# Optimization experiments

Measured on AMD Instinct MI355X. Metric: run time of the kernel, lower is better.

The kernel has to match this reference:

```python
import jax, jax.numpy as jnp
import numpy as np

EMBED_DIM = 1024
BATCH = 4
SEQ = 2048


def setup_inputs() -> dict:
    key = jax.random.key(0)
    ks = jax.random.split(key, 9)
    E = EMBED_DIM
    s = 1.0 / np.sqrt(E)
    inp = {
        "x": jax.random.normal(ks[0], (BATCH, SEQ, E), dtype=jnp.float32),
        "Wq": jax.random.uniform(ks[1], (E, E), jnp.float32, -s, s),
        "bq": jax.random.uniform(ks[2], (E,), jnp.float32, -s, s),
        "Wk": jax.random.uniform(ks[3], (E, E), jnp.float32, -s, s),
        "bk": jax.random.uniform(ks[4], (E,), jnp.float32, -s, s),
        "Wv": jax.random.uniform(ks[5], (E, E), jnp.float32, -s, s),
        "bv": jax.random.uniform(ks[6], (E,), jnp.float32, -s, s),
        "Wo": jax.random.uniform(ks[7], (E, E), jnp.float32, -s, s),
        "bo": jax.random.uniform(ks[8], (E,), jnp.float32, -s, s),
    }
    return inp


def reference(x, Wq, bq, Wk, bk, Wv, bv, Wo, bo):
    # x: [B, S, E]. Single-head attention over full embed_dim.
    scale = x.shape[-1] ** -0.5
    q = jnp.einsum("bse,ef->bsf", x, Wq.T) + bq
    k = jnp.einsum("bse,ef->bsf", x, Wk.T) + bk
    v = jnp.einsum("bse,ef->bsf", x, Wv.T) + bv
    scores = jnp.einsum("bqe,bke->bqk", q, k) * scale  # [B, S, S]
    attn = jax.nn.softmax(scores, axis=-1)             # dropout p=0 -> identity
    out = jnp.einsum("bqk,bke->bqe", attn, v)
    return jnp.einsum("bse,ef->bsf", out, Wo.T) + bo
```

## Files before the change

### kernel.cpp

```cpp
#include <hip/hip_runtime.h>
#include <hip/hip_bf16.h>


typedef __bf16 bf16_t;
typedef __bf16 bf16x8 __attribute__((ext_vector_type(8)));
typedef __bf16 bf16x4 __attribute__((ext_vector_type(4)));
typedef float  f32x16 __attribute__((ext_vector_type(16)));

__device__ __forceinline__ void async_copy16(const void* g, void* l) {
  __builtin_amdgcn_global_load_lds(
      (const __attribute__((address_space(1))) void*)g,
      (__attribute__((address_space(3))) void*)l, 16, 0, 0);
}

__device__ __forceinline__ void store_out(float* p, float v)  { *p = v; }
__device__ __forceinline__ void store_out(bf16_t* p, float v) { *p = (bf16_t)v; }

#define BM 128
#define BN 128
#define BKT 64

template <typename OutT, int NBIAS>
__global__ __launch_bounds__(256) void gemm_bt(
    const bf16_t* __restrict__ A, const bf16_t* __restrict__ B,
    OutT* __restrict__ C,
    const float* __restrict__ b0, const float* __restrict__ b1,
    const float* __restrict__ b2,
    int M, int N, int K, int lda, int ldb, int ldc, float scale,
    long long strideA, long long strideB, long long strideC) {
  const int z = blockIdx.z;
  A += (long long)z * strideA;
  B += (long long)z * strideB;
  C += (long long)z * strideC;

  int bx = blockIdx.x, by = blockIdx.y;
  {
    const int GX  = gridDim.x;
    const int id  = by * GX + bx;
    const int per = GX * 8;
    const int grp = id / per;
    const int rem = id - grp * per;
    by = grp * 8 + (rem & 7);
    bx = rem >> 3;
  }

  __shared__ __align__(16) bf16_t As[BM * BKT];
  __shared__ __align__(16) bf16_t Bs[BN * BKT];

  const int t    = threadIdx.x;
  const int lane = t & 63;
  const int w    = t >> 6;
  const int wm   = w & 1;
  const int wn   = w >> 1;
  const int tileM = by * BM;
  const int tileN = bx * BN;

  f32x16 acc[2][2] = {};

  for (int k0 = 0; k0 < K; k0 += BKT) {
#pragma unroll
    for (int i = 0; i < 4; ++i) {
      const int c   = t + 256 * i;
      const int row = c >> 3;
      const int cc  = c & 7;
      const int gcc = cc ^ (row & 7);
      const int ldsbase = ((t & ~63) + 256 * i) * 8;
      async_copy16(A + (long long)(tileM + row) * lda + k0 + gcc * 8, &As[ldsbase]);
      async_copy16(B + (long long)(tileN + row) * ldb + k0 + gcc * 8, &Bs[ldsbase]);
    }
    __syncthreads();

#pragma unroll
    for (int s = 0; s < 4; ++s) {
      const int kc = s + 4 * (lane >> 5);
      bf16x8 af[2], bfr[2];
#pragma unroll
      for (int ti = 0; ti < 2; ++ti) {
        const int row = wm * 64 + ti * 32 + (lane & 31);
        af[ti] = *(const bf16x8*)&As[row * BKT + ((kc ^ (row & 7)) * 8)];
      }
#pragma unroll
      for (int tj = 0; tj < 2; ++tj) {
        const int row = wn * 64 + tj * 32 + (lane & 31);
        bfr[tj] = *(const bf16x8*)&Bs[row * BKT + ((kc ^ (row & 7)) * 8)];
      }
#pragma unroll
      for (int ti = 0; ti < 2; ++ti)
#pragma unroll
        for (int tj = 0; tj < 2; ++tj)
          acc[ti][tj] = __builtin_amdgcn_mfma_f32_32x32x16_bf16(
              af[ti], bfr[tj], acc[ti][tj], 0, 0, 0);
    }
    __syncthreads();
  }

#pragma unroll
  for (int tj = 0; tj < 2; ++tj) {
    const int col = tileN + wn * 64 + tj * 32 + (lane & 31);
    float bv = 0.f;
    if (NBIAS == 1) bv = b0[col];
    if (NBIAS == 3) {
      const float* bp = col < 1024 ? b0 : (col < 2048 ? b1 : b2);
      bv = bp[col & 1023];
    }
#pragma unroll
    for (int ti = 0; ti < 2; ++ti) {
      const int rowb = tileM + wm * 64 + ti * 32 + 4 * (lane >> 5);
#pragma unroll
      for (int r = 0; r < 16; ++r) {
        const int row = rowb + (r & 3) + 8 * (r >> 2);
        store_out(&C[(long long)row * ldc + col], acc[ti][tj][r] * scale + bv);
      }
    }
  }
}

__global__ __launch_bounds__(256) void cast_all(
    const float4* __restrict__ w0, const float4* __restrict__ w1,
    const float4* __restrict__ w2, const float4* __restrict__ w3,
    const float4* __restrict__ x,
    bf16x4* __restrict__ wdst, bf16x4* __restrict__ xdst) {
  const int N4W = 1 << 18;
  const int id = blockIdx.x * 256 + threadIdx.x;
  const float4* src;
  bf16x4* dst;
  if (id < 4 * N4W) {
    const int z = id >> 18;
    src = (z == 0 ? w0 : z == 1 ? w1 : z == 2 ? w2 : w3) + (id & (N4W - 1));
    dst = wdst + id;
  } else {
    const int i = id - 4 * N4W;
    src = x + i;
    dst = xdst + i;
  }
  const float4 v = *src;
  bf16x4 o;
  o[0] = (bf16_t)v.x; o[1] = (bf16_t)v.y; o[2] = (bf16_t)v.z; o[3] = (bf16_t)v.w;
  *dst = o;
}

__global__ __launch_bounds__(256) void transpose_bf16(
    const bf16_t* __restrict__ in, bf16_t* __restrict__ out, int R, int C,
    int ldin, long long sIn, long long sOut) {
  in  += (long long)blockIdx.z * sIn;
  out += (long long)blockIdx.z * sOut;
  __shared__ bf16_t tile[32][33];
  const int tx = threadIdx.x, ty = threadIdx.y;
  const int x = blockIdx.x * 32 + tx;
  const int y0 = blockIdx.y * 32;
#pragma unroll
  for (int j = 0; j < 32; j += 8)
    tile[ty + j][tx] = in[(long long)(y0 + ty + j) * ldin + x];
  __syncthreads();
  const int x2 = y0 + tx;
  const int y2 = blockIdx.x * 32;
#pragma unroll
  for (int j = 0; j < 32; j += 8)
    out[(long long)(y2 + ty + j) * R + x2] = tile[tx][ty + j];
}

__global__ __launch_bounds__(256) void softmax_rows(
    const bf16_t* __restrict__ S, bf16_t* __restrict__ P, int cols) {
  const long long row = blockIdx.x;
  const bf16x8* inp = (const bf16x8*)(S + row * cols);
  bf16x8* outp      = (bf16x8*)(P + row * cols);
  const int t = threadIdx.x;
  const int w = t >> 6, lane = t & 63;

  const bf16x8 v = inp[t];
  float f[8];
#pragma unroll
  for (int j = 0; j < 8; ++j) f[j] = (float)v[j];

  float m = f[0];
#pragma unroll
  for (int j = 1; j < 8; ++j) m = fmaxf(m, f[j]);
#pragma unroll
  for (int off = 32; off > 0; off >>= 1) m = fmaxf(m, __shfl_xor(m, off));

  __shared__ float red[8];
  if (lane == 0) red[w] = m;
  __syncthreads();
  m = fmaxf(fmaxf(red[0], red[1]), fmaxf(red[2], red[3]));

  float e[8], sum = 0.f;
#pragma unroll
  for (int j = 0; j < 8; ++j) { e[j] = __expf(f[j] - m); sum += e[j]; }
#pragma unroll
  for (int off = 32; off > 0; off >>= 1) sum += __shfl_xor(sum, off);
  if (lane == 0) red[4 + w] = sum;
  __syncthreads();
  sum = red[4] + red[5] + red[6] + red[7];

  const float inv = 1.f / sum;
  bf16x8 o;
#pragma unroll
  for (int j = 0; j < 8; ++j) o[j] = (bf16_t)(e[j] * inv);
  outp[t] = o;
}

extern "C" void kernel_launch(void* const* d_in, const int* in_sizes, int n_in,
                              void* d_out, int out_size, void* d_ws, size_t ws_size,
                              hipStream_t stream) {
  const int E = 1024, S = 2048, B = 4;
  const int BS = B * S;

  const float* x  = (const float*)d_in[0];
  const float* Wq = (const float*)d_in[1];
  const float* bq = (const float*)d_in[2];
  const float* Wk = (const float*)d_in[3];
  const float* bk = (const float*)d_in[4];
  const float* Wv = (const float*)d_in[5];
  const float* bv = (const float*)d_in[6];
  const float* Wo = (const float*)d_in[7];
  const float* bo = (const float*)d_in[8];
  float* out = (float*)d_out;

  char* w = (char*)d_ws;
  const size_t MB = 1ull << 20;
  bf16_t* Wqkvb = (bf16_t*)(w + 0 * MB);
  bf16_t* Wob   = Wqkvb + 3 * E * E;
  bf16_t* xb    = (bf16_t*)(w + 8 * MB);
  bf16_t* QKVb  = (bf16_t*)(w + 24 * MB);
  bf16_t* VTb   = (bf16_t*)(w + 72 * MB);
  bf16_t* Sb    = (bf16_t*)(w + 88 * MB);
  bf16_t* Pb    = (bf16_t*)(w + 8 * MB);
  bf16_t* Ob    = (bf16_t*)(w + 40 * MB);

  {
    const int totalBlocks = ((4 << 18) + (1 << 21)) / 256;
    cast_all<<<totalBlocks, 256, 0, stream>>>(
        (const float4*)Wq, (const float4*)Wk, (const float4*)Wv,
        (const float4*)Wo, (const float4*)x, (bf16x4*)Wqkvb, (bf16x4*)xb);
  }

  gemm_bt<bf16_t, 3><<<dim3(3 * E / BN, BS / BM, 1), 256, 0, stream>>>(
      xb, Wqkvb, QKVb, bq, bk, bv,
      BS, 3 * E, E, E, E, 3 * E, 1.f, 0, 0, 0);

  transpose_bf16<<<dim3(E / 32, S / 32, B), dim3(32, 8), 0, stream>>>(
      QKVb + 2 * E, VTb, S, E, 3 * E, (long long)S * 3 * E, (long long)E * S);

  gemm_bt<bf16_t, 0><<<dim3(S / BN, S / BM, B), 256, 0, stream>>>(
      QKVb, QKVb + E, Sb, nullptr, nullptr, nullptr,
      S, S, E, 3 * E, 3 * E, S, 0.03125f,
      (long long)S * 3 * E, (long long)S * 3 * E, (long long)S * S);

  softmax_rows<<<BS, 256, 0, stream>>>(Sb, Pb, S);

  gemm_bt<bf16_t, 0><<<dim3(E / BN, S / BM, B), 256, 0, stream>>>(
      Pb, VTb, Ob, nullptr, nullptr, nullptr,
      S, E, S, S, S, E, 1.f,
      (long long)S * S, (long long)E * S, (long long)S * E);

  gemm_bt<float, 1><<<dim3(E / BN, BS / BM, 1), 256, 0, stream>>>(
      Ob, Wob, out, bo, nullptr, nullptr,
      BS, E, E, E, E, E, 1.f, 0, 0, 0);
}
```

Before: 302.2 us.

## Add 256x256 eight-wave double-buffered GEMM for QKV projection and QK^T

Adds a new GEMM kernel with 256x256 output tiles, 512 threads and 16x16x32 bf16 MFMAs. It double-buffers A and B tiles in LDS through async global-to-LDS copies, with explicit vmcnt waits. The inner loop is split into four MFMA phases separated by barriers, interleaves the next tile's loads between them, and raises wave priority around the MFMA bursts. The goal is more data reuse per tile and less exposed load latency for the two largest GEMMs. In exchange it uses about 128KB of LDS, so only one block fits per CU, and the grids become smaller (384 and 256 blocks), which may underfill the GPU.

```diff
diff --git a/kernel.cpp b/kernel.cpp
--- a/kernel.cpp
+++ b/kernel.cpp
@@ -6,6 +6,7 @@
 typedef __bf16 bf16x8 __attribute__((ext_vector_type(8)));
 typedef __bf16 bf16x4 __attribute__((ext_vector_type(4)));
 typedef float  f32x16 __attribute__((ext_vector_type(16)));
+typedef float  f32x4  __attribute__((ext_vector_type(4)));
 
 __device__ __forceinline__ void async_copy16(const void* g, void* l) {
   __builtin_amdgcn_global_load_lds(
@@ -13,12 +14,193 @@
       (__attribute__((address_space(3))) void*)l, 16, 0, 0);
 }
 
+__device__ __forceinline__ void wg_barrier() {
+  asm volatile("" ::: "memory");
+  __builtin_amdgcn_s_barrier();
+  asm volatile("" ::: "memory");
+}
+
+__device__ __forceinline__ f32x4 mfma16(bf16x8 a, bf16x8 b, f32x4 c) {
+  return __builtin_amdgcn_mfma_f32_16x16x32_bf16(a, b, c, 0, 0, 0);
+}
+
 __device__ __forceinline__ void store_out(float* p, float v)  { *p = v; }
 __device__ __forceinline__ void store_out(bf16_t* p, float v) { *p = (bf16_t)v; }
 
 #define BM 128
 #define BN 128
 #define BKT 64
+
+template <typename OutT, int NBIAS>
+__global__ __launch_bounds__(512, 2) void gemm256_bt(
+    const bf16_t* __restrict__ A, const bf16_t* __restrict__ B,
+    OutT* __restrict__ C,
+    const float* __restrict__ b0, const float* __restrict__ b1,
+    const float* __restrict__ b2,
+    int M, int N, int K, int lda, int ldb, int ldc, float scale,
+    long long strideA, long long strideB, long long strideC) {
+  const int z = blockIdx.z;
+  A += (long long)z * strideA;
+  B += (long long)z * strideB;
+  C += (long long)z * strideC;
+
+  int bx = blockIdx.x, by = blockIdx.y;
+  {
+    const int GX  = gridDim.x;
+    const int id  = by * GX + bx;
+    const int per = GX * 8;
+    const int grp = id / per;
+    const int rem = id - grp * per;
+    by = grp * 8 + (rem & 7);
+    bx = rem >> 3;
+  }
+
+  __shared__ __align__(16) bf16_t As[2 * 256 * 64];
+  __shared__ __align__(16) bf16_t Bs[2 * 256 * 64];
+
+  const int t    = threadIdx.x;
+  const int lane = t & 63;
+  const int w    = t >> 6;
+  const int wm   = w & 1;
+  const int wn   = w >> 1;
+  const int g    = lane >> 4;
+  const int l7   = lane & 7;
+  const int r15  = lane & 15;
+  const int tileM = by * 256;
+  const int tileN = bx * 256;
+
+  const int row0 = t >> 3;
+  const int gcc  = (t & 7) ^ (row0 & 7);
+  const int dstb = (t & ~63) * 8;
+
+  const int sw0 = ((0 + g) ^ l7) * 8;
+  const int sw1 = ((4 + g) ^ l7) * 8;
+  const int aRow = (wm * 128 + r15) * 64;
+  const int bRow = (wn * 64 + r15) * 64;
+
+  const int NT = K >> 6;
+
+  f32x4 acc[8][4] = {};
+
+  auto stageA = [&](int kt, int h) {
+    const int cb = (kt & 1) * 16384;
+    const bf16_t* src =
+        A + (long long)(tileM + h * 128 + row0) * lda + kt * 64 + gcc * 8;
+    bf16_t* dst = &As[cb + h * 8192 + dstb];
+    async_copy16(src, dst);
+    async_copy16(src + (long long)64 * lda, dst + 4096);
+  };
+  auto stageB = [&](int kt, int h) {
+    const int cb = (kt & 1) * 16384;
+    const bf16_t* src =
+        B + (long long)(tileN + h * 128 + row0) * ldb + kt * 64 + gcc * 8;
+    bf16_t* dst = &Bs[cb + h * 8192 + dstb];
+    async_copy16(src, dst);
+    async_copy16(src + (long long)64 * ldb, dst + 4096);
+  };
+
+  stageA(0, 0); stageA(0, 1); stageB(0, 0); stageB(0, 1);
+  stageA(1, 0); stageA(1, 1); stageB(1, 0); stageB(1, 1);
+  asm volatile("s_waitcnt vmcnt(8)" ::: "memory");
+  wg_barrier();
+
+  bf16x8 a[4][2], bq[2][2][2];
+
+  for (int kt = 0; kt < NT; ++kt) {
+    const int cb = (kt & 1) * 16384;
+    const int k2 = kt + 2;
+
+#pragma unroll
+    for (int i = 0; i < 4; ++i) {
+      a[i][0] = *(const bf16x8*)&As[cb + aRow + i * 1024 + sw0];
+      a[i][1] = *(const bf16x8*)&As[cb + aRow + i * 1024 + sw1];
+    }
+#pragma unroll
+    for (int j = 0; j < 2; ++j) {
+      bq[0][j][0] = *(const bf16x8*)&Bs[cb + bRow + j * 1024 + sw0];
+      bq[0][j][1] = *(const bf16x8*)&Bs[cb + bRow + j * 1024 + sw1];
+    }
+    wg_barrier();
+    __builtin_amdgcn_s_setprio(1);
+#pragma unroll
+    for (int i = 0; i < 4; ++i)
+#pragma unroll
+      for (int j = 0; j < 2; ++j) {
+        acc[i][j] = mfma16(a[i][0], bq[0][j][0], acc[i][j]);
+        acc[i][j] = mfma16(a[i][1], bq[0][j][1], acc[i][j]);
+      }
+    __builtin_amdgcn_s_setprio(0);
+    wg_barrier();
+
+#pragma unroll
+    for (int j = 0; j < 2; ++j) {
+      bq[1][j][0] = *(const bf16x8*)&Bs[cb + bRow + 2048 + j * 1024 + sw0];
+      bq[1][j][1] = *(const bf16x8*)&Bs[cb + bRow + 2048 + j * 1024 + sw1];
+    }
+    wg_barrier();
+    __builtin_amdgcn_s_setprio(1);
+#pragma unroll
+    for (int i = 0; i < 4; ++i)
+#pragma unroll
+      for (int j = 0; j < 2; ++j) {
+        acc[i][2 + j] = mfma16(a[i][0], bq[1][j][0], acc[i][2 + j]);
+        acc[i][2 + j] = mfma16(a[i][1], bq[1][j][1], acc[i][2 + j]);
+      }
+    __builtin_amdgcn_s_setprio(0);
+    wg_barrier();
+
+#pragma unroll
+    for (int i = 0; i < 4; ++i) {
+      a[i][0] = *(const bf16x8*)&As[cb + aRow + 4096 + i * 1024 + sw0];
+      a[i][1] = *(const bf16x8*)&As[cb + aRow + 4096 + i * 1024 + sw1];
+    }
+    if (k2 < NT) { stageB(k2, 0); stageB(k2, 1); }
+    wg_barrier();
+    __builtin_amdgcn_s_setprio(1);
+#pragma unroll
+    for (int i = 0; i < 4; ++i)
+#pragma unroll
+      for (int j = 0; j < 2; ++j) {
+        acc[4 + i][2 + j] = mfma16(a[i][0], bq[1][j][0], acc[4 + i][2 + j]);
+        acc[4 + i][2 + j] = mfma16(a[i][1], bq[1][j][1], acc[4 + i][2 + j]);
+      }
+    __builtin_amdgcn_s_setprio(0);
+    wg_barrier();
+
+    if (k2 < NT) { stageA(k2, 0); stageA(k2, 1); }
+    __builtin_amdgcn_s_setprio(1);
+#pragma unroll
+    for (int i = 0; i < 4; ++i)
+#pragma unroll
+      for (int j = 0; j < 2; ++j) {
+        acc[4 + i][j] = mfma16(a[i][0], bq[0][j][0], acc[4 + i][j]);
+        acc[4 + i][j] = mfma16(a[i][1], bq[0][j][1], acc[4 + i][j]);
+      }
+    __builtin_amdgcn_s_setprio(0);
+    if (k2 < NT) asm volatile("s_waitcnt vmcnt(8)" ::: "memory");
+    else         asm volatile("s_waitcnt vmcnt(0)" ::: "memory");
+    wg_barrier();
+  }
+
+#pragma unroll
+  for (int j = 0; j < 4; ++j) {
+    const int col = tileN + wn * 64 + j * 16 + r15;
+    float bv = 0.f;
+    if (NBIAS == 1) bv = b0[col];
+    if (NBIAS == 3) {
+      const float* bp = col < 1024 ? b0 : (col < 2048 ? b1 : b2);
+      bv = bp[col & 1023];
+    }
+#pragma unroll
+    for (int i = 0; i < 8; ++i) {
+      const int rowb = tileM + wm * 128 + i * 16 + g * 4;
+#pragma unroll
+      for (int r = 0; r < 4; ++r)
+        store_out(&C[(long long)(rowb + r) * ldc + col],
+                  acc[i][j][r] * scale + bv);
+    }
+  }
+}
 
 template <typename OutT, int NBIAS>
 __global__ __launch_bounds__(256) void gemm_bt(
@@ -234,14 +416,14 @@
         (const float4*)Wo, (const float4*)x, (bf16x4*)Wqkvb, (bf16x4*)xb);
   }
 
-  gemm_bt<bf16_t, 3><<<dim3(3 * E / BN, BS / BM, 1), 256, 0, stream>>>(
+  gemm256_bt<bf16_t, 3><<<dim3(3 * E / 256, BS / 256, 1), 512, 0, stream>>>(
       xb, Wqkvb, QKVb, bq, bk, bv,
       BS, 3 * E, E, E, E, 3 * E, 1.f, 0, 0, 0);
 
   transpose_bf16<<<dim3(E / 32, S / 32, B), dim3(32, 8), 0, stream>>>(
       QKVb + 2 * E, VTb, S, E, 3 * E, (long long)S * 3 * E, (long long)E * S);
 
-  gemm_bt<bf16_t, 0><<<dim3(S / BN, S / BM, B), 256, 0, stream>>>(
+  gemm256_bt<bf16_t, 0><<<dim3(S / 256, S / 256, B), 512, 0, stream>>>(
       QKVb, QKVb + E, Sb, nullptr, nullptr, nullptr,
       S, S, E, 3 * E, 3 * E, S, 0.03125f,
       (long long)S * 3 * E, (long long)S * 3 * E, (long long)S * S);
```

Result: slower. 313.2 us (+3.6%).
